# Kernel tuning notes

Measured on AMD Instinct MI355X. Metric: run time of the kernel, lower is better.

The kernel has to match this reference:

```python
import jax, jax.numpy as jnp
import numpy as np

PATCH_LENS = [8, 16, 24, 48]
MAX_P = 48
MIN_P = 8
TARGET = MAX_P // MIN_P  # 6 patches per region after repeat_interleave
N_EXP = len(PATCH_LENS)
D_MODEL = 512
TAU = 0.5


def _repeat_idx(plen):
    # Mirrors: patches.repeat_interleave(repeat+1, dim=1)[:, :TARGET]
    n = MAX_P // plen
    k = TARGET - n + 1  # repeat + 1
    idx = np.arange(TARGET) // k if k > 1 else np.arange(TARGET)
    return jnp.asarray(np.minimum(idx, n - 1), dtype=jnp.int32)


def _pos_emb(L, d):
    # PositionalEmbedding buffer (sin/cos), sliced to length L
    pos = np.arange(L, dtype=np.float64)[:, None]
    div = np.exp(np.arange(0, d, 2, dtype=np.float64) * -(np.log(10000.0) / d))
    pe = np.zeros((L, d), np.float32)
    pe[:, 0::2] = np.sin(pos * div).astype(np.float32)
    pe[:, 1::2] = np.cos(pos * div).astype(np.float32)
    return jnp.asarray(pe)


def setup_inputs() -> dict:
    key = jax.random.key(0)
    ks = jax.random.split(key, 8)
    B, C, S = 128, 32, 336
    N, R = B * C, S // MAX_P
    x = jax.random.normal(ks[0], (B, C, S), dtype=jnp.float32)
    u_noise = jax.random.uniform(ks[1], (N, R, N_EXP), dtype=jnp.float32)
    W1 = jax.random.normal(ks[2], (MAX_P, 64), dtype=jnp.float32) * 0.02
    b1 = jnp.zeros((64,), jnp.float32)
    W2 = jax.random.normal(ks[3], (64, N_EXP), dtype=jnp.float32) * 0.02
    b2 = jnp.zeros((N_EXP,), jnp.float32)
    W_emb0 = jax.random.normal(ks[4], (PATCH_LENS[0], D_MODEL), dtype=jnp.float32) * 0.02
    W_emb1 = jax.random.normal(ks[5], (PATCH_LENS[1], D_MODEL), dtype=jnp.float32) * 0.02
    W_emb2 = jax.random.normal(ks[6], (PATCH_LENS[2], D_MODEL), dtype=jnp.float32) * 0.02
    W_emb3 = jax.random.normal(ks[7], (PATCH_LENS[3], D_MODEL), dtype=jnp.float32) * 0.02
    return {"x": x, "u_noise": u_noise, "W1": W1, "b1": b1, "W2": W2, "b2": b2,
            "W_emb0": W_emb0, "W_emb1": W_emb1, "W_emb2": W_emb2, "W_emb3": W_emb3}


def reference(x, u_noise, W1, b1, W2, b2, W_emb0, W_emb1, W_emb2, W_emb3):
    B, C, S = x.shape
    R = S // MAX_P
    xr = x.reshape(B * C, R, MAX_P)                       # [N, R, 48]

    # Region-wise router MLP (vectorized over all regions)
    logits = jax.nn.relu(xr @ W1 + b1) @ W2 + b2          # [N, R, E]
    # Gumbel-softmax (tau=0.5, hard=True, straight-through)
    g = -jnp.log(-jnp.log(u_noise + 1e-10) + 1e-10)
    soft = jax.nn.softmax((logits + g) / TAU, axis=-1)
    hard = jax.nn.one_hot(jnp.argmax(soft, axis=-1), N_EXP, dtype=soft.dtype)
    cls_soft = hard + soft - jax.lax.stop_gradient(soft)  # [N, R, E]

    # Per-candidate-patch-length embedding, weighted combine (accumulate to cap memory)
    W_embs = [W_emb0, W_emb1, W_emb2, W_emb3]
    out = jnp.zeros((B * C, R, TARGET, D_MODEL), dtype=x.dtype)
    for i, plen in enumerate(PATCH_LENS):
        n = MAX_P // plen
        # unfold(step==size) == reshape; then repeat_interleave+slice == static gather
        patches = xr.reshape(B * C, R, n, plen)[:, :, _repeat_idx(plen), :]  # [N,R,T,plen]
        emb = patches @ W_embs[i]                          # [N, R, T, d]
        out = out + emb * cls_soft[..., i][..., None, None]

    x_patch = out.reshape(B * C, R * TARGET, D_MODEL)
    x_patch = x_patch + _pos_emb(R * TARGET, D_MODEL)[None]

    # torch.cat of per-region [N] argmaxes along dim 0 -> region-major flatten
    cls_pred = jnp.argmax(cls_soft, axis=-1).T.reshape(-1)  # [R*N]
    return x_patch, jnp.int32(C), cls_pred
```

## Files before the change

kernel.cpp:

```cpp
#include <hip/hip_runtime.h>
#include <math.h>


namespace {
constexpr int NROWS = 4096;
constexpr int SEQ   = 336;
constexpr int RREG  = 7;
constexpr int TGT   = 6;
constexpr int DM    = 512;
constexpr int DM4   = DM / 4;
constexpr int NEXP  = 4;
constexpr int NREG  = NROWS * RREG;
constexpr long long XP_ELEMS = (long long)NROWS * RREG * TGT * DM;
constexpr int PE_ELEMS = RREG * TGT * DM;
constexpr size_t WS_FLOATS = (size_t)PE_ELEMS + (size_t)NREG * 2;
}

typedef float v4f __attribute__((ext_vector_type(4)));
typedef float v2f __attribute__((ext_vector_type(2)));

__global__ void pe_kernel(float* __restrict__ pe) {
    int i = blockIdx.x * blockDim.x + threadIdx.x;
    if (i >= PE_ELEMS) return;
    int p = i / DM, d = i - p * DM;
    int j = d >> 1;
    double div = exp((double)(2 * j) * -(log(10000.0) / (double)DM));
    double a = (double)p * div;
    pe[i] = (d & 1) ? (float)cos(a) : (float)sin(a);
}

__device__ inline float pe_val(int p, int d) {
    int j = d >> 1;
    float div = __expf((float)(2 * j) * (-9.210340371976184f / 512.0f));
    float a = (float)p * div;
    return (d & 1) ? __cosf(a) : __sinf(a);
}

__global__ __launch_bounds__(256) void router_kernel(
    const float* __restrict__ x,  const float* __restrict__ un,
    const float* __restrict__ W1, const float* __restrict__ b1,
    const float* __restrict__ W2, const float* __restrict__ b2,
    v2f* __restrict__ ew, float* __restrict__ out)
{
    const int g = blockIdx.x * 256 + threadIdx.x;
    if (g >= NREG) return;
    const int n = g / RREG, r = g - n * RREG;

    float xv[48];
    const v4f* xr4 = reinterpret_cast<const v4f*>(x + (size_t)n * SEQ + r * 48);
    #pragma unroll
    for (int i = 0; i < 12; ++i) {
        v4f v = xr4[i];
        xv[4 * i + 0] = v.x; xv[4 * i + 1] = v.y;
        xv[4 * i + 2] = v.z; xv[4 * i + 3] = v.w;
    }

    float z0 = b2[0], z1 = b2[1], z2 = b2[2], z3 = b2[3];
    for (int j = 0; j < 64; ++j) {
        float h = b1[j];
        #pragma unroll
        for (int k = 0; k < 48; ++k) h = fmaf(xv[k], W1[k * 64 + j], h);
        h = fmaxf(h, 0.0f);
        z0 = fmaf(h, W2[j * NEXP + 0], z0);
        z1 = fmaf(h, W2[j * NEXP + 1], z1);
        z2 = fmaf(h, W2[j * NEXP + 2], z2);
        z3 = fmaf(h, W2[j * NEXP + 3], z3);
    }

    const float* ug = un + (size_t)g * NEXP;
    z0 = (z0 + -logf(-logf(ug[0] + 1e-10f) + 1e-10f)) / 0.5f;
    z1 = (z1 + -logf(-logf(ug[1] + 1e-10f) + 1e-10f)) / 0.5f;
    z2 = (z2 + -logf(-logf(ug[2] + 1e-10f) + 1e-10f)) / 0.5f;
    z3 = (z3 + -logf(-logf(ug[3] + 1e-10f) + 1e-10f)) / 0.5f;

    int e = 0; float zm = z0;
    if (z1 > zm) { zm = z1; e = 1; }
    if (z2 > zm) { zm = z2; e = 2; }
    if (z3 > zm) { zm = z3; e = 3; }
    float s = 1.0f / (((expf(z0 - zm) + expf(z1 - zm)) + expf(z2 - zm)) + expf(z3 - zm));
    float w = (1.0f + s) - s;

    v2f p; p.x = w; p.y = (float)e;
    ew[g] = p;
    out[(size_t)XP_ELEMS + 1 + (size_t)r * NROWS + n] = (float)e;
    if (g == 0) out[(size_t)XP_ELEMS] = 32.0f;
}

__global__ __launch_bounds__(256) void embed_kernel(
    const float* __restrict__ x,   const v2f* __restrict__ ew,
    const float* __restrict__ We0, const float* __restrict__ We1,
    const float* __restrict__ We2, const float* __restrict__ We3,
    const float* __restrict__ pe,  float* __restrict__ out)
{
    const int blk = blockIdx.x;
    const int n = blk / RREG;
    const int r = blk - n * RREG;
    const int tid = threadIdx.x;

    const v2f ewv = ew[blk];
    const float w = ewv.x;
    const int e = (int)ewv.y;
    const float* __restrict__ xr = x + (size_t)n * SEQ + r * 48;

    const int c4   = tid & 127;
    const int half = tid >> 7;
    v4f* __restrict__ outv = reinterpret_cast<v4f*>(out);
    const v4f* __restrict__ pev = reinterpret_cast<const v4f*>(pe);
    const size_t ob = ((size_t)n * (RREG * TGT) + (size_t)r * TGT) * DM4;
    const int pb = r * TGT * DM4;

    auto emit = [&](int t, const v4f& a) {
        v4f pv = pev[pb + t * DM4 + c4];
        v4f v;
        v.x = fmaf(a.x, w, pv.x);
        v.y = fmaf(a.y, w, pv.y);
        v.z = fmaf(a.z, w, pv.z);
        v.w = fmaf(a.w, w, pv.w);
        __builtin_nontemporal_store(v, &outv[ob + (size_t)t * DM4 + c4]);
    };
    auto fma4 = [](float xvv, const v4f& wv, v4f& a) {
        a.x = fmaf(xvv, wv.x, a.x);
        a.y = fmaf(xvv, wv.y, a.y);
        a.z = fmaf(xvv, wv.z, a.z);
        a.w = fmaf(xvv, wv.w, a.w);
    };
    const v4f zero4 = (v4f)(0.0f);

    if (e == 0) {
        const v4f* W = reinterpret_cast<const v4f*>(We0);
        v4f a0 = zero4, a1 = zero4, a2 = zero4;
        #pragma unroll
        for (int k = 0; k < 8; ++k) {
            v4f wv = W[k * DM4 + c4];
            fma4(xr[(half + 0) * 8 + k], wv, a0);
            fma4(xr[(half + 2) * 8 + k], wv, a1);
            fma4(xr[(half + 4) * 8 + k], wv, a2);
        }
        emit(half + 0, a0);
        emit(half + 2, a1);
        emit(half + 4, a2);
    } else if (e == 1) {
        const v4f* W = reinterpret_cast<const v4f*>(We1);
        v4f a0 = zero4, a1 = zero4;
        #pragma unroll
        for (int k = 0; k < 16; ++k) {
            v4f wv = W[k * DM4 + c4];
            fma4(xr[k],      wv, a0);
            fma4(xr[16 + k], wv, a1);
        }
        #pragma unroll
        for (int i = 0; i < 3; ++i) {
            int t = half + 2 * i;
            emit(t, (t < 4) ? a0 : a1);
        }
    } else if (e == 2) {
        const v4f* W = reinterpret_cast<const v4f*>(We2);
        v4f a0 = zero4, a1 = zero4;
        #pragma unroll
        for (int k = 0; k < 24; ++k) {
            v4f wv = W[k * DM4 + c4];
            fma4(xr[k],      wv, a0);
            fma4(xr[24 + k], wv, a1);
        }
        #pragma unroll
        for (int i = 0; i < 3; ++i) {
            int t = half + 2 * i;
            emit(t, (t < 5) ? a0 : a1);
        }
    } else {
        const v4f* W = reinterpret_cast<const v4f*>(We3);
        v4f a0 = zero4;
        #pragma unroll
        for (int k = 0; k < 48; ++k) {
            v4f wv = W[k * DM4 + c4];
            fma4(xr[k], wv, a0);
        }
        #pragma unroll
        for (int i = 0; i < 3; ++i) emit(half + 2 * i, a0);
    }
}

__global__ __launch_bounds__(256) void apk_fused_kernel(
    const float* __restrict__ x,   const float* __restrict__ un,
    const float* __restrict__ W1,  const float* __restrict__ b1,
    const float* __restrict__ W2,  const float* __restrict__ b2,
    const float* __restrict__ We0, const float* __restrict__ We1,
    const float* __restrict__ We2, const float* __restrict__ We3,
    float* __restrict__ out)
{
    const int blk = blockIdx.x;
    const int n = blk / RREG;
    const int r = blk - n * RREG;
    const int tid = threadIdx.x;

    __shared__ float sx[48];
    __shared__ float sh[64];
    __shared__ float sz[NEXP];
    __shared__ float s_w;
    __shared__ int   s_e;

    if (tid < 48) sx[tid] = x[(size_t)n * SEQ + r * 48 + tid];
    __syncthreads();
    if (tid < 64) {
        float h = b1[tid];
        #pragma unroll
        for (int k = 0; k < 48; ++k) h = fmaf(sx[k], W1[k * 64 + tid], h);
        sh[tid] = fmaxf(h, 0.0f);
    }
    __syncthreads();
    if (tid < NEXP) {
        float z = b2[tid];
        #pragma unroll
        for (int j = 0; j < 64; ++j) z = fmaf(sh[j], W2[j * NEXP + tid], z);
        float uu = un[(size_t)blk * NEXP + tid];
        float g = -logf(-logf(uu + 1e-10f) + 1e-10f);
        sz[tid] = (z + g) / 0.5f;
    }
    __syncthreads();
    if (tid == 0) {
        float z0 = sz[0], z1 = sz[1], z2 = sz[2], z3 = sz[3];
        int e = 0; float zm = z0;
        if (z1 > zm) { zm = z1; e = 1; }
        if (z2 > zm) { zm = z2; e = 2; }
        if (z3 > zm) { zm = z3; e = 3; }
        float s = 1.0f / (((expf(z0 - zm) + expf(z1 - zm)) + expf(z2 - zm)) + expf(z3 - zm));
        s_e = e;
        s_w = (1.0f + s) - s;
        out[(size_t)XP_ELEMS + 1 + (size_t)r * NROWS + n] = (float)e;
        if (blk == 0) out[(size_t)XP_ELEMS] = 32.0f;
    }
    __syncthreads();

    const int e = s_e;
    const float w = s_w;
    const int c4   = tid & 127;
    const int half = tid >> 7;
    v4f* __restrict__ outv = reinterpret_cast<v4f*>(out);
    const size_t ob = ((size_t)n * (RREG * TGT) + (size_t)r * TGT) * DM4;

    auto pe4 = [&](int t) -> v4f {
        v4f v;
        v.x = pe_val(r * TGT + t, 4 * c4 + 0);
        v.y = pe_val(r * TGT + t, 4 * c4 + 1);
        v.z = pe_val(r * TGT + t, 4 * c4 + 2);
        v.w = pe_val(r * TGT + t, 4 * c4 + 3);
        return v;
    };
    auto emit = [&](int t, const v4f& a) {
        v4f pv = pe4(t);
        v4f v;
        v.x = fmaf(a.x, w, pv.x);
        v.y = fmaf(a.y, w, pv.y);
        v.z = fmaf(a.z, w, pv.z);
        v.w = fmaf(a.w, w, pv.w);
        __builtin_nontemporal_store(v, &outv[ob + (size_t)t * DM4 + c4]);
    };
    auto fma4 = [](float xv, const v4f& wv, v4f& a) {
        a.x = fmaf(xv, wv.x, a.x);
        a.y = fmaf(xv, wv.y, a.y);
        a.z = fmaf(xv, wv.z, a.z);
        a.w = fmaf(xv, wv.w, a.w);
    };
    const v4f zero4 = (v4f)(0.0f);

    if (e == 0) {
        const v4f* W = reinterpret_cast<const v4f*>(We0);
        v4f a0 = zero4, a1 = zero4, a2 = zero4;
        #pragma unroll
        for (int k = 0; k < 8; ++k) {
            v4f wv = W[k * DM4 + c4];
            fma4(sx[(half + 0) * 8 + k], wv, a0);
            fma4(sx[(half + 2) * 8 + k], wv, a1);
            fma4(sx[(half + 4) * 8 + k], wv, a2);
        }
        emit(half + 0, a0); emit(half + 2, a1); emit(half + 4, a2);
    } else if (e == 1) {
        const v4f* W = reinterpret_cast<const v4f*>(We1);
        v4f a0 = zero4, a1 = zero4;
        #pragma unroll
        for (int k = 0; k < 16; ++k) {
            v4f wv = W[k * DM4 + c4];
            fma4(sx[k], wv, a0); fma4(sx[16 + k], wv, a1);
        }
        #pragma unroll
        for (int i = 0; i < 3; ++i) { int t = half + 2 * i; emit(t, (t < 4) ? a0 : a1); }
    } else if (e == 2) {
        const v4f* W = reinterpret_cast<const v4f*>(We2);
        v4f a0 = zero4, a1 = zero4;
        #pragma unroll
        for (int k = 0; k < 24; ++k) {
            v4f wv = W[k * DM4 + c4];
            fma4(sx[k], wv, a0); fma4(sx[24 + k], wv, a1);
        }
        #pragma unroll
        for (int i = 0; i < 3; ++i) { int t = half + 2 * i; emit(t, (t < 5) ? a0 : a1); }
    } else {
        const v4f* W = reinterpret_cast<const v4f*>(We3);
        v4f a0 = zero4;
        #pragma unroll
        for (int k = 0; k < 48; ++k) { v4f wv = W[k * DM4 + c4]; fma4(sx[k], wv, a0); }
        #pragma unroll
        for (int i = 0; i < 3; ++i) emit(half + 2 * i, a0);
    }
}

extern "C" void kernel_launch(void* const* d_in, const int* in_sizes, int n_in,
                              void* d_out, int out_size, void* d_ws, size_t ws_size,
                              hipStream_t stream) {
    const float* x   = (const float*)d_in[0];
    const float* un  = (const float*)d_in[1];
    const float* W1  = (const float*)d_in[2];
    const float* b1  = (const float*)d_in[3];
    const float* W2  = (const float*)d_in[4];
    const float* b2  = (const float*)d_in[5];
    const float* We0 = (const float*)d_in[6];
    const float* We1 = (const float*)d_in[7];
    const float* We2 = (const float*)d_in[8];
    const float* We3 = (const float*)d_in[9];
    float* out = (float*)d_out;

    if (ws_size >= WS_FLOATS * sizeof(float)) {
        float* pe = (float*)d_ws;
        v2f* ew = reinterpret_cast<v2f*>((float*)d_ws + PE_ELEMS);
        pe_kernel<<<(PE_ELEMS + 255) / 256, 256, 0, stream>>>(pe);
        router_kernel<<<(NREG + 255) / 256, 256, 0, stream>>>(
            x, un, W1, b1, W2, b2, ew, out);
        embed_kernel<<<NREG, 256, 0, stream>>>(
            x, ew, We0, We1, We2, We3, pe, out);
    } else {
        apk_fused_kernel<<<NREG, 256, 0, stream>>>(
            x, un, W1, b1, W2, b2, We0, We1, We2, We3, out);
    }
}
```

Baseline: 446.2 us.

## Restructure embed kernel to process 16 rows per block with register-resident weights

The embedding kernel now launches one 512-thread block per 16 rows instead of one block per region. Each thread owns one output column, holds every expert's weight column in registers, and caches the positional table in shared memory. The aim is to amortise weight and positional loads across many regions. In exchange it uses heavy registers (96 weight floats plus 48 x values), a large shared-memory table (about 84KB), only 256 blocks, and scalar instead of vector nontemporal stores, so occupancy and store efficiency may suffer.

```diff
diff --git a/kernel.cpp b/kernel.cpp
--- a/kernel.cpp
+++ b/kernel.cpp
@@ -8,12 +8,13 @@
 constexpr int RREG  = 7;
 constexpr int TGT   = 6;
 constexpr int DM    = 512;
-constexpr int DM4   = DM / 4;
 constexpr int NEXP  = 4;
 constexpr int NREG  = NROWS * RREG;
 constexpr long long XP_ELEMS = (long long)NROWS * RREG * TGT * DM;
 constexpr int PE_ELEMS = RREG * TGT * DM;
 constexpr size_t WS_FLOATS = (size_t)PE_ELEMS + (size_t)NREG * 2;
+constexpr int ROWS = 16;
+constexpr int EMB_BLOCKS = NROWS / ROWS;
 }
 
 typedef float v4f __attribute__((ext_vector_type(4)));
@@ -86,101 +87,93 @@
     if (g == 0) out[(size_t)XP_ELEMS] = 32.0f;
 }
 
-__global__ __launch_bounds__(256) void embed_kernel(
+__global__ __launch_bounds__(512) void embed2_kernel(
     const float* __restrict__ x,   const v2f* __restrict__ ew,
     const float* __restrict__ We0, const float* __restrict__ We1,
     const float* __restrict__ We2, const float* __restrict__ We3,
     const float* __restrict__ pe,  float* __restrict__ out)
 {
-    const int blk = blockIdx.x;
-    const int n = blk / RREG;
-    const int r = blk - n * RREG;
-    const int tid = threadIdx.x;
-
-    const v2f ewv = ew[blk];
-    const float w = ewv.x;
-    const int e = (int)ewv.y;
-    const float* __restrict__ xr = x + (size_t)n * SEQ + r * 48;
-
-    const int c4   = tid & 127;
-    const int half = tid >> 7;
-    v4f* __restrict__ outv = reinterpret_cast<v4f*>(out);
-    const v4f* __restrict__ pev = reinterpret_cast<const v4f*>(pe);
-    const size_t ob = ((size_t)n * (RREG * TGT) + (size_t)r * TGT) * DM4;
-    const int pb = r * TGT * DM4;
-
-    auto emit = [&](int t, const v4f& a) {
-        v4f pv = pev[pb + t * DM4 + c4];
-        v4f v;
-        v.x = fmaf(a.x, w, pv.x);
-        v.y = fmaf(a.y, w, pv.y);
-        v.z = fmaf(a.z, w, pv.z);
-        v.w = fmaf(a.w, w, pv.w);
-        __builtin_nontemporal_store(v, &outv[ob + (size_t)t * DM4 + c4]);
-    };
-    auto fma4 = [](float xvv, const v4f& wv, v4f& a) {
-        a.x = fmaf(xvv, wv.x, a.x);
-        a.y = fmaf(xvv, wv.y, a.y);
-        a.z = fmaf(xvv, wv.z, a.z);
-        a.w = fmaf(xvv, wv.w, a.w);
-    };
-    const v4f zero4 = (v4f)(0.0f);
-
-    if (e == 0) {
-        const v4f* W = reinterpret_cast<const v4f*>(We0);
-        v4f a0 = zero4, a1 = zero4, a2 = zero4;
-        #pragma unroll
-        for (int k = 0; k < 8; ++k) {
-            v4f wv = W[k * DM4 + c4];
-            fma4(xr[(half + 0) * 8 + k], wv, a0);
-            fma4(xr[(half + 2) * 8 + k], wv, a1);
-            fma4(xr[(half + 4) * 8 + k], wv, a2);
+    const int d  = threadIdx.x;
+    const int n0 = blockIdx.x * ROWS;
+
+    __shared__ float s_pe[PE_ELEMS];
+    for (int i = d; i < PE_ELEMS; i += 512) s_pe[i] = pe[i];
+
+    float w0[8], w1[16], w2[24], w3[48];
+    #pragma unroll
+    for (int k = 0; k < 8;  ++k) w0[k] = We0[k * DM + d];
+    #pragma unroll
+    for (int k = 0; k < 16; ++k) w1[k] = We1[k * DM + d];
+    #pragma unroll
+    for (int k = 0; k < 24; ++k) w2[k] = We2[k * DM + d];
+    #pragma unroll
+    for (int k = 0; k < 48; ++k) w3[k] = We3[k * DM + d];
+    __syncthreads();
+
+    for (int ni = 0; ni < ROWS; ++ni) {
+        const int n = n0 + ni;
+        const float* __restrict__ xrow = x + (size_t)n * SEQ;
+
+        for (int r = 0; r < RREG; ++r) {
+            const v2f p = ew[(size_t)n * RREG + r];
+            const float w = p.x;
+            const int   e = (int)p.y;
+            const float* __restrict__ sx = xrow + r * 48;
+            float xv[48];
+            #pragma unroll
+            for (int k = 0; k < 48; ++k) xv[k] = sx[k];
+
+            const size_t ob = ((size_t)n * RREG + r) * TGT * DM + d;
+            const int pb = r * TGT * DM + d;
+
+            if (e == 0) {
+                float a[6] = {0.f, 0.f, 0.f, 0.f, 0.f, 0.f};
+                #pragma unroll
+                for (int k = 0; k < 8; ++k) {
+                    const float wv = w0[k];
+                    #pragma unroll
+                    for (int q = 0; q < 6; ++q) a[q] = fmaf(xv[q * 8 + k], wv, a[q]);
+                }
+                #pragma unroll
+                for (int t = 0; t < 6; ++t)
+                    out[ob + (size_t)t * DM] = fmaf(a[t], w, s_pe[pb + t * DM]);
+            } else if (e == 1) {
+                float a0 = 0.f, a1 = 0.f;
+                #pragma unroll
+                for (int k = 0; k < 16; ++k) {
+                    const float wv = w1[k];
+                    a0 = fmaf(xv[k],      wv, a0);
+                    a1 = fmaf(xv[16 + k], wv, a1);
+                }
+                #pragma unroll
+                for (int t = 0; t < 6; ++t)
+                    out[ob + (size_t)t * DM] =
+                        fmaf((t < 4) ? a0 : a1, w, s_pe[pb + t * DM]);
+            } else if (e == 2) {
+                float a0 = 0.f, a1 = 0.f;
+                #pragma unroll
+                for (int k = 0; k < 24; ++k) {
+                    const float wv = w2[k];
+                    a0 = fmaf(xv[k],      wv, a0);
+                    a1 = fmaf(xv[24 + k], wv, a1);
+                }
+                #pragma unroll
+                for (int t = 0; t < 6; ++t)
+                    out[ob + (size_t)t * DM] =
+                        fmaf((t < 5) ? a0 : a1, w, s_pe[pb + t * DM]);
+            } else {
+                float a0 = 0.f;
+                #pragma unroll
+                for (int k = 0; k < 48; ++k) a0 = fmaf(xv[k], w3[k], a0);
+                #pragma unroll
+                for (int t = 0; t < 6; ++t)
+                    out[ob + (size_t)t * DM] = fmaf(a0, w, s_pe[pb + t * DM]);
+            }
         }
-        emit(half + 0, a0);
-        emit(half + 2, a1);
-        emit(half + 4, a2);
-    } else if (e == 1) {
-        const v4f* W = reinterpret_cast<const v4f*>(We1);
-        v4f a0 = zero4, a1 = zero4;
-        #pragma unroll
-        for (int k = 0; k < 16; ++k) {
-            v4f wv = W[k * DM4 + c4];
-            fma4(xr[k],      wv, a0);
-            fma4(xr[16 + k], wv, a1);
-        }
-        #pragma unroll
-        for (int i = 0; i < 3; ++i) {
-            int t = half + 2 * i;
-            emit(t, (t < 4) ? a0 : a1);
-        }
-    } else if (e == 2) {
-        const v4f* W = reinterpret_cast<const v4f*>(We2);
-        v4f a0 = zero4, a1 = zero4;
-        #pragma unroll
-        for (int k = 0; k < 24; ++k) {
-            v4f wv = W[k * DM4 + c4];
-            fma4(xr[k],      wv, a0);
-            fma4(xr[24 + k], wv, a1);
-        }
-        #pragma unroll
-        for (int i = 0; i < 3; ++i) {
-            int t = half + 2 * i;
-            emit(t, (t < 5) ? a0 : a1);
-        }
-    } else {
-        const v4f* W = reinterpret_cast<const v4f*>(We3);
-        v4f a0 = zero4;
-        #pragma unroll
-        for (int k = 0; k < 48; ++k) {
-            v4f wv = W[k * DM4 + c4];
-            fma4(xr[k], wv, a0);
-        }
-        #pragma unroll
-        for (int i = 0; i < 3; ++i) emit(half + 2 * i, a0);
-    }
-}
-
-__global__ __launch_bounds__(256) void apk_fused_kernel(
+    }
+}
+
+__global__ __launch_bounds__(256) void fused_fb_kernel(
     const float* __restrict__ x,   const float* __restrict__ un,
     const float* __restrict__ W1,  const float* __restrict__ b1,
     const float* __restrict__ W2,  const float* __restrict__ b2,
@@ -224,8 +217,7 @@
         if (z2 > zm) { zm = z2; e = 2; }
         if (z3 > zm) { zm = z3; e = 3; }
         float s = 1.0f / (((expf(z0 - zm) + expf(z1 - zm)) + expf(z2 - zm)) + expf(z3 - zm));
-        s_e = e;
-        s_w = (1.0f + s) - s;
+        s_e = e; s_w = (1.0f + s) - s;
         out[(size_t)XP_ELEMS + 1 + (size_t)r * NROWS + n] = (float)e;
         if (blk == 0) out[(size_t)XP_ELEMS] = 32.0f;
     }
@@ -233,74 +225,42 @@
 
     const int e = s_e;
     const float w = s_w;
-    const int c4   = tid & 127;
-    const int half = tid >> 7;
-    v4f* __restrict__ outv = reinterpret_cast<v4f*>(out);
-    const size_t ob = ((size_t)n * (RREG * TGT) + (size_t)r * TGT) * DM4;
-
-    auto pe4 = [&](int t) -> v4f {
-        v4f v;
-        v.x = pe_val(r * TGT + t, 4 * c4 + 0);
-        v.y = pe_val(r * TGT + t, 4 * c4 + 1);
-        v.z = pe_val(r * TGT + t, 4 * c4 + 2);
-        v.w = pe_val(r * TGT + t, 4 * c4 + 3);
-        return v;
-    };
-    auto emit = [&](int t, const v4f& a) {
-        v4f pv = pe4(t);
-        v4f v;
-        v.x = fmaf(a.x, w, pv.x);
-        v.y = fmaf(a.y, w, pv.y);
-        v.z = fmaf(a.z, w, pv.z);
-        v.w = fmaf(a.w, w, pv.w);
-        __builtin_nontemporal_store(v, &outv[ob + (size_t)t * DM4 + c4]);
-    };
-    auto fma4 = [](float xv, const v4f& wv, v4f& a) {
-        a.x = fmaf(xv, wv.x, a.x);
-        a.y = fmaf(xv, wv.y, a.y);
-        a.z = fmaf(xv, wv.z, a.z);
-        a.w = fmaf(xv, wv.w, a.w);
-    };
-    const v4f zero4 = (v4f)(0.0f);
-
-    if (e == 0) {
-        const v4f* W = reinterpret_cast<const v4f*>(We0);
-        v4f a0 = zero4, a1 = zero4, a2 = zero4;
-        #pragma unroll
-        for (int k = 0; k < 8; ++k) {
-            v4f wv = W[k * DM4 + c4];
-            fma4(sx[(half + 0) * 8 + k], wv, a0);
-            fma4(sx[(half + 2) * 8 + k], wv, a1);
-            fma4(sx[(half + 4) * 8 + k], wv, a2);
+    const int d = tid;
+    for (int rep = 0; rep < 2; ++rep) {
+        const int dd = d + rep * 256;
+        const size_t ob = ((size_t)n * RREG + r) * TGT * DM + dd;
+        float acc[6] = {0.f, 0.f, 0.f, 0.f, 0.f, 0.f};
+        if (e == 0) {
+            for (int k = 0; k < 8; ++k) {
+                float wv = We0[k * DM + dd];
+                #pragma unroll
+                for (int q = 0; q < 6; ++q) acc[q] = fmaf(sx[q * 8 + k], wv, acc[q]);
+            }
+        } else if (e == 1) {
+            for (int k = 0; k < 16; ++k) {
+                float wv = We1[k * DM + dd];
+                acc[0] = fmaf(sx[k], wv, acc[0]);
+                acc[4] = fmaf(sx[16 + k], wv, acc[4]);
+            }
+            acc[1] = acc[2] = acc[3] = acc[0]; acc[5] = acc[4];
+        } else if (e == 2) {
+            for (int k = 0; k < 24; ++k) {
+                float wv = We2[k * DM + dd];
+                acc[0] = fmaf(sx[k], wv, acc[0]);
+                acc[5] = fmaf(sx[24 + k], wv, acc[5]);
+            }
+            acc[1] = acc[2] = acc[3] = acc[4] = acc[0];
+        } else {
+            for (int k = 0; k < 48; ++k) {
+                float wv = We3[k * DM + dd];
+                acc[0] = fmaf(sx[k], wv, acc[0]);
+            }
+            acc[1] = acc[2] = acc[3] = acc[4] = acc[5] = acc[0];
         }
-        emit(half + 0, a0); emit(half + 2, a1); emit(half + 4, a2);
-    } else if (e == 1) {
-        const v4f* W = reinterpret_cast<const v4f*>(We1);
-        v4f a0 = zero4, a1 = zero4;
-        #pragma unroll
-        for (int k = 0; k < 16; ++k) {
-            v4f wv = W[k * DM4 + c4];
-            fma4(sx[k], wv, a0); fma4(sx[16 + k], wv, a1);
-        }
-        #pragma unroll
-        for (int i = 0; i < 3; ++i) { int t = half + 2 * i; emit(t, (t < 4) ? a0 : a1); }
-    } else if (e == 2) {
-        const v4f* W = reinterpret_cast<const v4f*>(We2);
-        v4f a0 = zero4, a1 = zero4;
-        #pragma unroll
-        for (int k = 0; k < 24; ++k) {
-            v4f wv = W[k * DM4 + c4];
-            fma4(sx[k], wv, a0); fma4(sx[24 + k], wv, a1);
-        }
-        #pragma unroll
-        for (int i = 0; i < 3; ++i) { int t = half + 2 * i; emit(t, (t < 5) ? a0 : a1); }
-    } else {
-        const v4f* W = reinterpret_cast<const v4f*>(We3);
-        v4f a0 = zero4;
-        #pragma unroll
-        for (int k = 0; k < 48; ++k) { v4f wv = W[k * DM4 + c4]; fma4(sx[k], wv, a0); }
-        #pragma unroll
-        for (int i = 0; i < 3; ++i) emit(half + 2 * i, a0);
+        #pragma unroll
+        for (int t = 0; t < 6; ++t)
+            out[ob + (size_t)t * DM] =
+                fmaf(acc[t], w, pe_val(r * TGT + t, dd));
     }
 }
 
@@ -325,10 +285,10 @@
         pe_kernel<<<(PE_ELEMS + 255) / 256, 256, 0, stream>>>(pe);
         router_kernel<<<(NREG + 255) / 256, 256, 0, stream>>>(
             x, un, W1, b1, W2, b2, ew, out);
-        embed_kernel<<<NREG, 256, 0, stream>>>(
+        embed2_kernel<<<EMB_BLOCKS, 512, 0, stream>>>(
             x, ew, We0, We1, We2, We3, pe, out);
     } else {
-        apk_fused_kernel<<<NREG, 256, 0, stream>>>(
+        fused_fb_kernel<<<NREG, 256, 0, stream>>>(
             x, un, W1, b1, W2, b2, We0, We1, We2, We3, out);
     }
 }
```

New measurement: 439.4 us. Within noise of the previous version (-1.5%).
